# Optimization experiments

Hardware: AMD Instinct MI355X
Metric: run time of the kernel (lower is better)

## Reference

```python
import jax, jax.numpy as jnp
import numpy as np
from jax import lax


def _b3_kernel_2d(dtype=jnp.float32):
    k1 = jnp.array([1.0 / 16.0, 1.0 / 4.0, 3.0 / 8.0, 1.0 / 4.0, 1.0 / 16.0], dtype=dtype)
    return jnp.outer(k1, k1)  # (5, 5)


def _dilated_b3_conv(x, kernel_2d, dilation):
    # PyTorch Conv2d(kernel_size=5, dilation=d, padding=2*d, padding_mode='reflect')
    pad = 2 * dilation
    xp = jnp.pad(x, ((0, 0), (0, 0), (pad, pad), (pad, pad)), mode='reflect')
    k = kernel_2d[None, None, :, :]  # (O=1, I=1, 5, 5)
    return lax.conv_general_dilated(
        xp, k,
        window_strides=(1, 1),
        padding='VALID',
        rhs_dilation=(dilation, dilation),
        dimension_numbers=('NCHW', 'OIHW', 'NCHW'),
    )


def setup_inputs() -> dict:
    key = jax.random.key(0)
    B, H, W = 16, 1024, 1024
    x = jax.random.normal(key, (B, 1, H, W), dtype=jnp.float32)
    kernel_2d = _b3_kernel_2d(jnp.float32)
    return {"x": x, "kernel_2d": kernel_2d, "n_scales": 5}


def reference(x, kernel_2d, n_scales):
    # a trous starlet transform: detail_j = c_j - c_{j+1}; last channel = coarse
    detail_scales = []
    coarse = x
    for scale_idx in range(n_scales - 1):
        dilation = 2 ** scale_idx
        next_coarse = _dilated_b3_conv(coarse, kernel_2d, dilation)
        detail_scales.append(coarse - next_coarse)
        coarse = next_coarse
    all_scales = detail_scales + [coarse]
    return jnp.concatenate(all_scales, axis=1)  # (B, n_scales, H, W)
```

## Files before the change

### kernel.cpp

```cpp
#include <hip/hip_runtime.h>

#define TX 64
#define TY 64

template<int D>
__global__ __launch_bounds__(256)
void starlet_scale(const float* __restrict__ in, long in_bs,
                   float* __restrict__ det,      long det_bs,
                   float* __restrict__ coa,      long coa_bs)
{
    constexpr int H = 1024, W = 1024;
    constexpr int R  = 2 * D;
    constexpr int LW = TX + 2 * R;
    constexpr int LH = TY + 2 * R;
    constexpr int LS = LW + 1;

    __shared__ float tile[LH * LS];
    __shared__ float htmp[LH * TX];

    const int tid = threadIdx.x;
    const int bx  = blockIdx.x * TX;
    const int by  = blockIdx.y * TY;
    const int b   = blockIdx.z;

    const float* __restrict__ inp = in + (long)b * in_bs;

    const float k0 = 0.0625f;
    const float k1 = 0.25f;
    const float k2 = 0.375f;

    for (int i = tid; i < LH * LW; i += 256) {
        int ly = i / LW;
        int lx = i - ly * LW;
        int gy = by - R + ly;
        gy = (gy < 0) ? -gy : ((gy >= H) ? (2 * H - 2 - gy) : gy);
        int gx = bx - R + lx;
        gx = (gx < 0) ? -gx : ((gx >= W) ? (2 * W - 2 - gx) : gx);
        tile[ly * LS + lx] = inp[(long)gy * W + gx];
    }
    __syncthreads();

    for (int i = tid; i < LH * TX; i += 256) {
        int r = i >> 6;
        int x = i & (TX - 1);
        const float* t = &tile[r * LS + x];
        htmp[i] = k0 * (t[0] + t[4 * D]) + k1 * (t[D] + t[3 * D]) + k2 * t[2 * D];
    }
    __syncthreads();

    for (int i = tid; i < TY * TX; i += 256) {
        int y = i >> 6;
        int x = i & (TX - 1);
        const float* h = &htmp[y * TX + x];
        float conv = k0 * (h[0] + h[4 * D * TX])
                   + k1 * (h[D * TX] + h[3 * D * TX])
                   + k2 * h[2 * D * TX];
        float center = tile[(y + R) * LS + (x + R)];
        long gidx = (long)(by + y) * W + (bx + x);
        det[(long)b * det_bs + gidx] = center - conv;
        coa[(long)b * coa_bs + gidx] = conv;
    }
}

extern "C" void kernel_launch(void* const* d_in, const int* in_sizes, int n_in,
                              void* d_out, int out_size, void* d_ws, size_t ws_size,
                              hipStream_t stream) {
    const float* x = (const float*)d_in[0];
    float* out = (float*)d_out;
    float* ws  = (float*)d_ws;

    const long HW = 1024L * 1024L;
    const long OB = 5 * HW;

    dim3 grid(1024 / TX, 1024 / TY, 16);
    dim3 block(256);

    starlet_scale<1><<<grid, block, 0, stream>>>(x, HW, out + 0 * HW, OB, ws, HW);
    starlet_scale<2><<<grid, block, 0, stream>>>(ws, HW, out + 1 * HW, OB, out + 4 * HW, OB);
    starlet_scale<4><<<grid, block, 0, stream>>>(out + 4 * HW, OB, out + 2 * HW, OB, ws, HW);
    starlet_scale<8><<<grid, block, 0, stream>>>(ws, HW, out + 3 * HW, OB, out + 4 * HW, OB);
}
```

Before: 512.7 us.

## Fuse starlet scale pairs into two kernels with halo recompute and float4 access

Merges the four per-scale launches into two kernels that each compute two consecutive dilation levels inside one tile, keeping the intermediate coarse image in shared memory and recomputing the wider halo. This removes two full global round trips of the intermediate coarse arrays. Loads and stores now use float4, and interior tiles take a fast path that skips reflect-index math. The cost is larger shared-memory tiles with extra redundant halo computation, which may lower occupancy, plus more intricate indexing that has to match reflect padding exactly.

```diff
diff --git a/kernel.cpp b/kernel.cpp
--- a/kernel.cpp
+++ b/kernel.cpp
@@ -1,64 +1,218 @@
 #include <hip/hip_runtime.h>
 
-#define TX 64
-#define TY 64
-
-template<int D>
-__global__ __launch_bounds__(256)
-void starlet_scale(const float* __restrict__ in, long in_bs,
-                   float* __restrict__ det,      long det_bs,
-                   float* __restrict__ coa,      long coa_bs)
+#define WD 1024
+#define HT 1024
+
+__device__ __forceinline__ int refl(int g, int n) {
+    g = (g < 0) ? -g : g;
+    return (g >= n) ? (2 * n - 2 - g) : g;
+}
+
+__device__ __forceinline__ float4 conv5(float4 a, float4 b, float4 c, float4 d, float4 e) {
+    float4 o;
+    o.x = 0.0625f * (a.x + e.x) + 0.25f * (b.x + d.x) + 0.375f * c.x;
+    o.y = 0.0625f * (a.y + e.y) + 0.25f * (b.y + d.y) + 0.375f * c.y;
+    o.z = 0.0625f * (a.z + e.z) + 0.25f * (b.z + d.z) + 0.375f * c.z;
+    o.w = 0.0625f * (a.w + e.w) + 0.25f * (b.w + d.w) + 0.375f * c.w;
+    return o;
+}
+
+__device__ __forceinline__ float4 sub4(float4 a, float4 b) {
+    return make_float4(a.x - b.x, a.y - b.y, a.z - b.z, a.w - b.w);
+}
+
+__global__ __launch_bounds__(256) void starlet01(
+    const float* __restrict__ in, long in_bs,
+    float* __restrict__ det0, float* __restrict__ det1, long ob,
+    float* __restrict__ c2, long c2_bs)
 {
-    constexpr int H = 1024, W = 1024;
-    constexpr int R  = 2 * D;
-    constexpr int LW = TX + 2 * R;
-    constexpr int LH = TY + 2 * R;
-    constexpr int LS = LW + 1;
-
-    __shared__ float tile[LH * LS];
-    __shared__ float htmp[LH * TX];
-
+    __shared__ float A[76 * 80];
+    __shared__ float B[76 * 72];
     const int tid = threadIdx.x;
-    const int bx  = blockIdx.x * TX;
-    const int by  = blockIdx.y * TY;
-    const int b   = blockIdx.z;
-
+    const int bx = blockIdx.x * 64, by = blockIdx.y * 64;
+    const int b = blockIdx.z;
     const float* __restrict__ inp = in + (long)b * in_bs;
-
-    const float k0 = 0.0625f;
-    const float k1 = 0.25f;
-    const float k2 = 0.375f;
-
-    for (int i = tid; i < LH * LW; i += 256) {
-        int ly = i / LW;
-        int lx = i - ly * LW;
-        int gy = by - R + ly;
-        gy = (gy < 0) ? -gy : ((gy >= H) ? (2 * H - 2 - gy) : gy);
-        int gx = bx - R + lx;
-        gx = (gx < 0) ? -gx : ((gx >= W) ? (2 * W - 2 - gx) : gx);
-        tile[ly * LS + lx] = inp[(long)gy * W + gx];
-    }
-    __syncthreads();
-
-    for (int i = tid; i < LH * TX; i += 256) {
-        int r = i >> 6;
-        int x = i & (TX - 1);
-        const float* t = &tile[r * LS + x];
-        htmp[i] = k0 * (t[0] + t[4 * D]) + k1 * (t[D] + t[3 * D]) + k2 * t[2 * D];
-    }
-    __syncthreads();
-
-    for (int i = tid; i < TY * TX; i += 256) {
-        int y = i >> 6;
-        int x = i & (TX - 1);
-        const float* h = &htmp[y * TX + x];
-        float conv = k0 * (h[0] + h[4 * D * TX])
-                   + k1 * (h[D * TX] + h[3 * D * TX])
-                   + k2 * h[2 * D * TX];
-        float center = tile[(y + R) * LS + (x + R)];
-        long gidx = (long)(by + y) * W + (bx + x);
-        det[(long)b * det_bs + gidx] = center - conv;
-        coa[(long)b * coa_bs + gidx] = conv;
+    const float K0 = 0.0625f, K1 = 0.25f, K2 = 0.375f;
+
+    const bool interior = (bx >= 8) && (bx + 72 <= WD) && (by >= 6) && (by + 70 <= HT);
+
+    if (interior) {
+        const float4* __restrict__ src =
+            (const float4*)(inp + (long)(by - 6) * WD + (bx - 8));
+        float4* __restrict__ dst = (float4*)A;
+        #pragma unroll 2
+        for (int i = tid; i < 76 * 20; i += 256) {
+            int r = i / 20, c = i - r * 20;
+            dst[i] = src[(long)r * (WD / 4) + c];
+        }
+    } else {
+        for (int i = tid; i < 76 * 80; i += 256) {
+            int r = i / 80, c = i - r * 80;
+            int gy = refl(by - 6 + r, HT);
+            int gx = refl(bx - 8 + c, WD);
+            A[i] = inp[(long)gy * WD + gx];
+        }
+    }
+    __syncthreads();
+
+    for (int i = tid; i < 76 * 18; i += 256) {
+        int r = i / 18, cg = i - r * 18;
+        int c = cg * 4;
+        const float* a = &A[r * 80 + c];
+        float4 f0 = *(const float4*)(a);
+        float4 f1 = *(const float4*)(a + 4);
+        float4 f2 = *(const float4*)(a + 8);
+        float4 o;
+        o.x = K0 * (f0.z + f1.z) + K1 * (f0.w + f1.y) + K2 * f1.x;
+        o.y = K0 * (f0.w + f1.w) + K1 * (f1.x + f1.z) + K2 * f1.y;
+        o.z = K0 * (f1.x + f2.x) + K1 * (f1.y + f1.w) + K2 * f1.z;
+        o.w = K0 * (f1.y + f2.y) + K1 * (f1.z + f2.x) + K2 * f1.w;
+        *(float4*)&B[r * 72 + c] = o;
+    }
+    __syncthreads();
+
+    for (int i = tid; i < 72 * 18; i += 256) {
+        int r = i / 18, cg = i - r * 18;
+        int c = cg * 4;
+        float4 b0 = *(const float4*)&B[(r + 0) * 72 + c];
+        float4 b1 = *(const float4*)&B[(r + 1) * 72 + c];
+        float4 b2 = *(const float4*)&B[(r + 2) * 72 + c];
+        float4 b3 = *(const float4*)&B[(r + 3) * 72 + c];
+        float4 b4 = *(const float4*)&B[(r + 4) * 72 + c];
+        float4 c1v = conv5(b0, b1, b2, b3, b4);
+        float4* aslot = (float4*)&A[(r + 2) * 80 + c + 4];
+        float4 xv = *aslot;
+        if (r >= 4 && r < 68 && c >= 4 && c < 68) {
+            int gy = by + r - 4, gx = bx + c - 4;
+            *(float4*)&det0[(long)b * ob + (long)gy * WD + gx] = sub4(xv, c1v);
+        }
+        *aslot = c1v;
+    }
+    __syncthreads();
+
+    for (int i = tid; i < 72 * 16; i += 256) {
+        int r = i / 16, cg = i - r * 16;
+        int c = cg * 4;
+        const float* a = &A[(r + 2) * 80 + c + 4];
+        float4 f0 = *(const float4*)(a);
+        float4 f1 = *(const float4*)(a + 4);
+        float4 f2 = *(const float4*)(a + 8);
+        float4 o;
+        o.x = K0 * (f0.x + f2.x) + K1 * (f0.z + f1.z) + K2 * f1.x;
+        o.y = K0 * (f0.y + f2.y) + K1 * (f0.w + f1.w) + K2 * f1.y;
+        o.z = K0 * (f0.z + f2.z) + K1 * (f1.x + f2.x) + K2 * f1.z;
+        o.w = K0 * (f0.w + f2.w) + K1 * (f1.y + f2.y) + K2 * f1.w;
+        *(float4*)&B[r * 64 + c] = o;
+    }
+    __syncthreads();
+
+    for (int i = tid; i < 64 * 16; i += 256) {
+        int r = i / 16, cg = i - r * 16;
+        int c = cg * 4;
+        float4 b0 = *(const float4*)&B[(r + 0) * 64 + c];
+        float4 b2 = *(const float4*)&B[(r + 2) * 64 + c];
+        float4 b4 = *(const float4*)&B[(r + 4) * 64 + c];
+        float4 b6 = *(const float4*)&B[(r + 6) * 64 + c];
+        float4 b8 = *(const float4*)&B[(r + 8) * 64 + c];
+        float4 cv = conv5(b0, b2, b4, b6, b8);
+        float4 c1v = *(const float4*)&A[(r + 6) * 80 + c + 8];
+        long gidx = (long)(by + r) * WD + (bx + c);
+        *(float4*)&det1[(long)b * ob + gidx] = sub4(c1v, cv);
+        *(float4*)&c2[(long)b * c2_bs + gidx] = cv;
+    }
+}
+
+__global__ __launch_bounds__(256) void starlet23(
+    const float* __restrict__ in, long in_bs,
+    float* __restrict__ det2, float* __restrict__ det3, long ob,
+    float* __restrict__ c4, long c4_bs)
+{
+    __shared__ float A[80 * 112];
+    __shared__ float B[80 * 96];
+    const int tid = threadIdx.x;
+    const int bx = blockIdx.x * 64, by = blockIdx.y * 32;
+    const int b = blockIdx.z;
+    const float* __restrict__ inp = in + (long)b * in_bs;
+
+    const bool interior = (bx >= 24) && (bx + 88 <= WD) && (by >= 24) && (by + 56 <= HT);
+
+    if (interior) {
+        const float4* __restrict__ src =
+            (const float4*)(inp + (long)(by - 24) * WD + (bx - 24));
+        float4* __restrict__ dst = (float4*)A;
+        #pragma unroll 2
+        for (int i = tid; i < 80 * 28; i += 256) {
+            int r = i / 28, c = i - r * 28;
+            dst[i] = src[(long)r * (WD / 4) + c];
+        }
+    } else {
+        for (int i = tid; i < 80 * 112; i += 256) {
+            int r = i / 112, c = i - r * 112;
+            int gy = refl(by - 24 + r, HT);
+            int gx = refl(bx - 24 + c, WD);
+            A[i] = inp[(long)gy * WD + gx];
+        }
+    }
+    __syncthreads();
+
+    for (int i = tid; i < 80 * 24; i += 256) {
+        int r = i / 24, cg = i - r * 24;
+        int c = cg * 4;
+        const float* a = &A[r * 112 + c];
+        float4 g0 = *(const float4*)(a);
+        float4 g1 = *(const float4*)(a + 4);
+        float4 g2 = *(const float4*)(a + 8);
+        float4 g3 = *(const float4*)(a + 12);
+        float4 g4 = *(const float4*)(a + 16);
+        *(float4*)&B[r * 96 + c] = conv5(g0, g1, g2, g3, g4);
+    }
+    __syncthreads();
+
+    for (int i = tid; i < 64 * 24; i += 256) {
+        int r = i / 24, cg = i - r * 24;
+        int c = cg * 4;
+        float4 b0 = *(const float4*)&B[(r + 0) * 96 + c];
+        float4 b1 = *(const float4*)&B[(r + 4) * 96 + c];
+        float4 b2 = *(const float4*)&B[(r + 8) * 96 + c];
+        float4 b3 = *(const float4*)&B[(r + 12) * 96 + c];
+        float4 b4 = *(const float4*)&B[(r + 16) * 96 + c];
+        float4 c3v = conv5(b0, b1, b2, b3, b4);
+        float4* aslot = (float4*)&A[(r + 8) * 112 + c + 8];
+        float4 xv = *aslot;
+        if (r >= 16 && r < 48 && c >= 16 && c < 80) {
+            int gy = by + r - 16, gx = bx + c - 16;
+            *(float4*)&det2[(long)b * ob + (long)gy * WD + gx] = sub4(xv, c3v);
+        }
+        *aslot = c3v;
+    }
+    __syncthreads();
+
+    for (int i = tid; i < 64 * 16; i += 256) {
+        int r = i / 16, cg = i - r * 16;
+        int c = cg * 4;
+        const float* a = &A[(r + 8) * 112 + c + 8];
+        float4 g0 = *(const float4*)(a);
+        float4 g1 = *(const float4*)(a + 8);
+        float4 g2 = *(const float4*)(a + 16);
+        float4 g3 = *(const float4*)(a + 24);
+        float4 g4 = *(const float4*)(a + 32);
+        *(float4*)&B[r * 64 + c] = conv5(g0, g1, g2, g3, g4);
+    }
+    __syncthreads();
+
+    for (int i = tid; i < 32 * 16; i += 256) {
+        int r = i / 16, cg = i - r * 16;
+        int c = cg * 4;
+        float4 b0 = *(const float4*)&B[(r + 0) * 64 + c];
+        float4 b1 = *(const float4*)&B[(r + 8) * 64 + c];
+        float4 b2 = *(const float4*)&B[(r + 16) * 64 + c];
+        float4 b3 = *(const float4*)&B[(r + 24) * 64 + c];
+        float4 b4 = *(const float4*)&B[(r + 32) * 64 + c];
+        float4 c4v = conv5(b0, b1, b2, b3, b4);
+        float4 c3v = *(const float4*)&A[(r + 24) * 112 + c + 24];
+        long gidx = (long)(by + r) * WD + (bx + c);
+        *(float4*)&det3[(long)b * ob + gidx] = sub4(c3v, c4v);
+        *(float4*)&c4[(long)b * c4_bs + gidx] = c4v;
     }
 }
 
@@ -67,16 +221,14 @@
                               hipStream_t stream) {
     const float* x = (const float*)d_in[0];
     float* out = (float*)d_out;
-    float* ws  = (float*)d_ws;
+    float* ws = (float*)d_ws;
 
     const long HW = 1024L * 1024L;
     const long OB = 5 * HW;
-
-    dim3 grid(1024 / TX, 1024 / TY, 16);
-    dim3 block(256);
-
-    starlet_scale<1><<<grid, block, 0, stream>>>(x, HW, out + 0 * HW, OB, ws, HW);
-    starlet_scale<2><<<grid, block, 0, stream>>>(ws, HW, out + 1 * HW, OB, out + 4 * HW, OB);
-    starlet_scale<4><<<grid, block, 0, stream>>>(out + 4 * HW, OB, out + 2 * HW, OB, ws, HW);
-    starlet_scale<8><<<grid, block, 0, stream>>>(ws, HW, out + 3 * HW, OB, out + 4 * HW, OB);
-}
+    dim3 blk(256);
+
+    starlet01<<<dim3(16, 16, 16), blk, 0, stream>>>(
+        x, HW, out + 0 * HW, out + 1 * HW, OB, ws, HW);
+    starlet23<<<dim3(16, 32, 16), blk, 0, stream>>>(
+        ws, HW, out + 2 * HW, out + 3 * HW, OB, out + 4 * HW, OB);
+}
```

Result: no change. 521.0 us (+1.6%).
